# Performance work log

Hardware: AMD Instinct MI355X
Metric: run time of the kernel (lower is better)

The kernel has to match this reference:

```python
import jax, jax.numpy as jnp
import numpy as np

B, T, E, H = 2, 2048, 768, 12
DH = E // H  # per-head attention dim
EPS = 1e-5


def setup_inputs() -> dict:
    key = jax.random.key(0)
    ks = jax.random.split(key, 12)
    s = 0.02
    return {
        "x": jax.random.normal(ks[0], (B, T, E), dtype=jnp.float32),
        # stacked per-head projection weights: [H, E, DH], biases [H, DH]
        "Wq": jax.random.normal(ks[1], (H, E, DH), dtype=jnp.float32) * s,
        "bq": jax.random.normal(ks[2], (H, DH), dtype=jnp.float32) * s,
        "Wk": jax.random.normal(ks[3], (H, E, DH), dtype=jnp.float32) * s,
        "bk": jax.random.normal(ks[4], (H, DH), dtype=jnp.float32) * s,
        "Wv": jax.random.normal(ks[5], (H, E, DH), dtype=jnp.float32) * s,
        "bv": jax.random.normal(ks[6], (H, DH), dtype=jnp.float32) * s,
        "Wo": jax.random.normal(ks[7], (E, E), dtype=jnp.float32) * s,
        "bo": jax.random.normal(ks[8], (E,), dtype=jnp.float32) * s,
        "gamma": jnp.ones((E,), dtype=jnp.float32),
        "beta": jnp.zeros((E,), dtype=jnp.float32),
    }


def reference(x, Wq, bq, Wk, bk, Wv, bv, Wo, bo, gamma, beta):
    # per-head projections (heads stacked on axis h)
    q = jnp.einsum("bte,hed->bhtd", x, Wq) + bq[None, :, None, :]
    k = jnp.einsum("bte,hed->bhtd", x, Wk) + bk[None, :, None, :]
    v = jnp.einsum("bte,hed->bhtd", x, Wv) + bv[None, :, None, :]

    scores = jnp.einsum("bhtd,bhsd->bhts", q, k) / jnp.sqrt(jnp.float32(DH))
    causal = jnp.tril(jnp.ones((T, T), dtype=bool))  # True = keep
    scores = jnp.where(causal[None, None], scores, -jnp.inf)
    attn = jax.nn.softmax(scores, axis=-1)
    o = jnp.einsum("bhts,bhsd->bhtd", attn, v)  # [B,H,T,DH]

    # concat heads in head order -> [B,T,E]
    concat = jnp.transpose(o, (0, 2, 1, 3)).reshape(B, T, E)
    proj = concat @ Wo + bo

    # LayerNorm(proj) then residual add
    mu = jnp.mean(proj, axis=-1, keepdims=True)
    var = jnp.mean((proj - mu) ** 2, axis=-1, keepdims=True)
    normed = (proj - mu) * jax.lax.rsqrt(var + EPS) * gamma + beta
    return x + normed
```

## Files before the change

### kernel.cpp

```cpp
#include <hip/hip_runtime.h>
#include <stdint.h>

#define NROWS 4096
#define EMB   768
#define NQKV  2304
#define TSEQ  2048
#define NHEAD 12
#define NBH   24

typedef unsigned short u16;
typedef u16  ushort4v __attribute__((ext_vector_type(4)));
typedef u16  ushort8 __attribute__((ext_vector_type(8)));
typedef __bf16 bf16x8 __attribute__((ext_vector_type(8)));
typedef float f32x4 __attribute__((ext_vector_type(4)));

typedef const __attribute__((address_space(1))) void* gas_ptr;
typedef __attribute__((address_space(3))) void* las_ptr;

__device__ __forceinline__ u16 f2bf(float f) {
  union { float f; uint32_t u; } v; v.f = f;
  uint32_t u = v.u;
  return (u16)((u + 0x7fffu + ((u >> 16) & 1u)) >> 16);
}
__device__ __forceinline__ float bf2f(u16 u) {
  union { uint32_t u; float f; } v; v.u = ((uint32_t)u) << 16;
  return v.f;
}
__device__ __forceinline__ uint32_t cvtpk(float lo, float hi) {
  uint32_t r;
  asm("v_cvt_pk_bf16_f32 %0, %1, %2" : "=v"(r) : "v"(lo), "v"(hi));
  return r;
}

#define VMCNT0 asm volatile("s_waitcnt vmcnt(0)" ::: "memory")
#define LGKM0  asm volatile("s_waitcnt lgkmcnt(0)" ::: "memory")
#define SBAR   __builtin_amdgcn_s_barrier()
#define SCHED0 __builtin_amdgcn_sched_barrier(0)

__global__ __launch_bounds__(256) void k_pack(const float* __restrict__ x, u16* __restrict__ xb,
                                              const float* __restrict__ Wq, const float* __restrict__ Wk,
                                              const float* __restrict__ Wv, u16* __restrict__ wt,
                                              const float* __restrict__ Wo, u16* __restrict__ wot,
                                              uint32_t* __restrict__ cnt, uint32_t* __restrict__ tbl) {
  int bid = blockIdx.x, tid = threadIdx.x;
  if (bid == 0) {
    if (tid < 8) cnt[tid] = 0;
    if (tid >= 64 && tid < 144) {
      int p = tid - 64;
      int myqb = 0, myc = 0, k = 0;
      for (int qb = 0; qb < 32; ++qb) {
        int nch = (qb + 8) >> 3;
        for (int c = 0; c < nch; ++c) { if (k == p) { myqb = qb; myc = c; } ++k; }
      }
      int t0 = myc * 8;
      int t1 = (myqb + 1 < t0 + 8) ? myqb + 1 : t0 + 8;
      int mylen = t1 - t0, myid = myqb * 4 + myc;
      int rank = 0;
      for (int qb = 0; qb < 32; ++qb) {
        int nch = (qb + 8) >> 3;
        for (int c = 0; c < nch; ++c) {
          int u0 = c * 8;
          int u1 = (qb + 1 < u0 + 8) ? qb + 1 : u0 + 8;
          int l = u1 - u0, id = qb * 4 + c;
          if (l > mylen || (l == mylen && id < myid)) ++rank;
        }
      }
      tbl[rank] = (uint32_t)myqb | ((uint32_t)t0 << 8) | ((uint32_t)t1 << 16)
                | ((uint32_t)myc << 24) | (myqb <= 7 ? 0x80000000u : 0u);
    }
  }
  if (bid < 1536) {
    int i = bid * 2048 + tid * 8;
    float4 a = *(const float4*)(x + i);
    float4 b = *(const float4*)(x + i + 4);
    uint4 o;
    o.x = cvtpk(a.x, a.y); o.y = cvtpk(a.z, a.w);
    o.z = cvtpk(b.x, b.y); o.w = cvtpk(b.z, b.w);
    *(uint4*)(xb + i) = o;
    return;
  }
  __shared__ u16 lds[64][68];
  if (bid < 1968) {
    int t = bid - 1536;
    int sel = t / 144, rest = t - sel * 144;
    int h = rest / 12, ec = rest - h * 12;
    const float* W = sel == 0 ? Wq : (sel == 1 ? Wk : Wv);
    const float* src = W + ((size_t)(h * EMB + ec * 64) * 64);
    int e = tid >> 2, d0 = (tid & 3) * 16;
#pragma unroll
    for (int j = 0; j < 4; ++j) {
      float4 v = *(const float4*)(src + (size_t)e * 64 + d0 + 4 * j);
      ushort4v pk;
      uint32_t w0 = cvtpk(v.x, v.y), w1 = cvtpk(v.z, v.w);
      pk[0] = (u16)(w0 & 0xffff); pk[1] = (u16)(w0 >> 16);
      pk[2] = (u16)(w1 & 0xffff); pk[3] = (u16)(w1 >> 16);
      *(ushort4v*)(&lds[e][d0 + 4 * j]) = pk;
    }
    __syncthreads();
    int d = tid >> 2, e0 = (tid & 3) * 16;
    ushort8 o0, o1;
#pragma unroll
    for (int j = 0; j < 8; ++j) { o0[j] = lds[e0 + j][d]; o1[j] = lds[e0 + 8 + j][d]; }
    int n = sel * EMB + h * 64 + d;
    u16* dst = wt + (size_t)n * EMB + ec * 64 + e0;
    *(ushort8*)dst = o0;
    *(ushort8*)(dst + 8) = o1;
  } else {
    int t = bid - 1968;
    int er = t / 12, nc = t - er * 12;
    int e = tid >> 2, n0 = (tid & 3) * 16;
#pragma unroll
    for (int j = 0; j < 4; ++j) {
      float4 v = *(const float4*)(Wo + (size_t)(er * 64 + e) * EMB + nc * 64 + n0 + 4 * j);
      ushort4v pk;
      uint32_t w0 = cvtpk(v.x, v.y), w1 = cvtpk(v.z, v.w);
      pk[0] = (u16)(w0 & 0xffff); pk[1] = (u16)(w0 >> 16);
      pk[2] = (u16)(w1 & 0xffff); pk[3] = (u16)(w1 >> 16);
      *(ushort4v*)(&lds[e][n0 + 4 * j]) = pk;
    }
    __syncthreads();
    int n = tid >> 2, e0 = (tid & 3) * 16;
    ushort8 o0, o1;
#pragma unroll
    for (int j = 0; j < 8; ++j) { o0[j] = lds[e0 + j][n]; o1[j] = lds[e0 + 8 + j][n]; }
    u16* dst = wot + (size_t)(nc * 64 + n) * EMB + er * 64 + e0;
    *(ushort8*)dst = o0;
    *(ushort8*)(dst + 8) = o1;
  }
}

template<int BM, int BN, int OUT_MODE>
__global__ __launch_bounds__(256) void k_gemm(const u16* __restrict__ A, const u16* __restrict__ Bt,
                                              const float* __restrict__ b0, const float* __restrict__ b1,
                                              const float* __restrict__ b2, void* __restrict__ Cout,
                                              u16* __restrict__ vtout, int M, int N, int K) {
  constexpr int MR = BM / 32, NR = BN / 32;
  __shared__ u16 lds_a[BM * 64];
  __shared__ u16 lds_b[BN * 64];
  int tid = threadIdx.x;
  int w = tid >> 6, lane = tid & 63;
  int wr = w >> 1, wc = w & 1;
  int m0 = blockIdx.x * BM, n0 = blockIdx.y * BN;
  int lrow = lane & 15, g = lane >> 4;

  f32x4 zero = {0.f, 0.f, 0.f, 0.f};
  f32x4 acc[MR][NR];
  for (int m = 0; m < MR; ++m) for (int n = 0; n < NR; ++n) acc[m][n] = zero;

  int l8 = lane >> 3, c8 = lane & 7;

  for (int k0 = 0; k0 < K; k0 += 64) {
#pragma unroll
    for (int i = 0; i < BM / 32; ++i) {
      int row = w * (BM / 4) + 8 * i + l8;
      int c16 = c8 ^ (row & 7);
      const u16* ga = A + (size_t)(m0 + row) * K + k0 + c16 * 8;
      __builtin_amdgcn_global_load_lds((gas_ptr)ga, (las_ptr)(lds_a + (w * (BM / 4) + 8 * i) * 64), 16, 0, 0);
    }
#pragma unroll
    for (int i = 0; i < BN / 32; ++i) {
      int row = w * (BN / 4) + 8 * i + l8;
      int c16 = c8 ^ (row & 7);
      const u16* gb = Bt + (size_t)(n0 + row) * K + k0 + c16 * 8;
      __builtin_amdgcn_global_load_lds((gas_ptr)gb, (las_ptr)(lds_b + (w * (BN / 4) + 8 * i) * 64), 16, 0, 0);
    }
    __syncthreads();
    bf16x8 af[MR][2], bfr[NR][2];
#pragma unroll
    for (int m = 0; m < MR; ++m)
#pragma unroll
      for (int kc = 0; kc < 2; ++kc) {
        int row = wr * (BM / 2) + m * 16 + lrow;
        int ch = (kc * 4 + g) ^ (row & 7);
        af[m][kc] = *(const bf16x8*)(lds_a + row * 64 + ch * 8);
      }
#pragma unroll
    for (int n = 0; n < NR; ++n)
#pragma unroll
      for (int kc = 0; kc < 2; ++kc) {
        int row = wc * (BN / 2) + n * 16 + lrow;
        int ch = (kc * 4 + g) ^ (row & 7);
        bfr[n][kc] = *(const bf16x8*)(lds_b + row * 64 + ch * 8);
      }
#pragma unroll
    for (int kc = 0; kc < 2; ++kc)
#pragma unroll
      for (int m = 0; m < MR; ++m)
#pragma unroll
        for (int n = 0; n < NR; ++n)
          acc[m][n] = __builtin_amdgcn_mfma_f32_16x16x32_bf16(af[m][kc], bfr[n][kc], acc[m][n], 0, 0, 0);
    __syncthreads();
  }

#pragma unroll
  for (int m = 0; m < MR; ++m)
#pragma unroll
    for (int n = 0; n < NR; ++n) {
      int col = n0 + wc * (BN / 2) + n * 16 + lrow;
      float bcol;
      if (OUT_MODE == 1) bcol = b0[col];
      else {
        int sel = col >= 1536 ? 2 : (col >= 768 ? 1 : 0);
        const float* bs = sel == 0 ? b0 : (sel == 1 ? b1 : b2);
        bcol = bs[col - sel * EMB];
      }
      int row0 = m0 + wr * (BM / 2) + m * 16 + 4 * g;
      if (OUT_MODE == 2 && col >= 2 * EMB) {
        int c = col - 2 * EMB;
        int hh = c >> 6, d = c & 63;
        int bb = row0 >> 11, t = row0 & 2047;
        int y = bb * NHEAD + hh;
        ushort4v pk;
#pragma unroll
        for (int r = 0; r < 4; ++r) pk[r] = f2bf(acc[m][n][r] + bcol);
        *(ushort4v*)(vtout + (size_t)(y * 64 + d) * TSEQ + t) = pk;
      } else {
#pragma unroll
        for (int r = 0; r < 4; ++r) {
          int row = row0 + r;
          float v = acc[m][n][r] + bcol;
          if (OUT_MODE == 1) ((float*)Cout)[(size_t)row * N + col] = v;
          else               ((u16*)Cout)[(size_t)row * N + col] = f2bf(v);
        }
      }
    }
}

__global__ __launch_bounds__(256, 4) void k_attn(const u16* __restrict__ qkv, const u16* __restrict__ vt,
                                                 u16* __restrict__ aout, uint32_t* __restrict__ cnt,
                                                 const uint32_t* __restrict__ tbl,
                                                 u16* __restrict__ pO, float* __restrict__ pL) {
  __shared__ u16 kbuf[64 * 64];
  __shared__ u16 vbuf[2][64 * 64];
  __shared__ u16 pbuf[4][16 * 64];
  __shared__ int task_s;
  int tid = threadIdx.x;
  int w = tid >> 6, lane = tid & 63;
  int ql = lane & 15, g = lane >> 4;
  int xcd = blockIdx.x & 7;
  const float sc2 = 0.18033688f;
  u16* pw = &pbuf[w][0];
  int swz = (ql & 7) << 3;
  int l8 = lane >> 3, c8 = lane & 7;

  for (;;) {
    if (tid == 0) task_s = (int)atomicAdd(&cnt[xcd], 1u);
    __syncthreads();
    int tau = task_s;
    __syncthreads();
    if (tau >= 240) break;

    int rank = tau / 3, yl = tau - rank * 3;
    uint32_t te = tbl[rank];
    int qb = te & 0xff, t0 = (te >> 8) & 0xff, t1ex = (te >> 16) & 0xff, cslot = (te >> 24) & 0x7f;
    bool direct = (te >> 31) != 0;

    int y = xcd * 3 + yl;
    int b = y / NHEAD, h = y - b * NHEAD;
    int qrow0w = qb * 64 + w * 16;
    int qg = qrow0w + ql;

    const u16* qp = qkv + (size_t)(b * TSEQ + qg) * NQKV + h * 64;
    bf16x8 bq0 = *(const bf16x8*)(qp + g * 8);
    bf16x8 bq1 = *(const bf16x8*)(qp + 32 + g * 8);

    const u16* kst = qkv + (size_t)(b * TSEQ) * NQKV + EMB + h * 64;
    const u16* vst = vt + (size_t)y * 64 * TSEQ;

    f32x4 zero = {0.f, 0.f, 0.f, 0.f};
    f32x4 o[4]; for (int n = 0; n < 4; ++n) o[n] = zero;
    float lr = 0.f;

    auto STAGE_K = [&](int t_) {
#pragma unroll
      for (int i = 0; i < 2; ++i) {
        int row = i * 32 + 8 * w + l8;
        int c16 = c8 ^ (row & 7);
        const u16* gk = kst + (size_t)(t_ * 64 + row) * NQKV + c16 * 8;
        __builtin_amdgcn_global_load_lds((gas_ptr)gk, (las_ptr)(&kbuf[(i * 32 + 8 * w) * 64]), 16, 0, 0);
      }
    };
    auto STAGE_V = [&](int bi, int t_) {
#pragma unroll
      for (int i = 0; i < 2; ++i) {
        int row = i * 32 + 8 * w + l8;
        int c16 = c8 ^ (row & 7);
        const u16* gv = vst + (size_t)row * TSEQ + t_ * 64 + c16 * 8;
        __builtin_amdgcn_global_load_lds((gas_ptr)gv, (las_ptr)(&vbuf[bi][(i * 32 + 8 * w) * 64]), 16, 0, 0);
      }
    };

    STAGE_K(t0);
    STAGE_V(t0 & 1, t0);
    for (int t = t0; t < t1ex; ++t) {
      VMCNT0;
      SBAR;

      f32x4 st[4];
#pragma unroll
      for (int sblk = 0; sblk < 4; ++sblk) {
        int row = sblk * 16 + ql;
        bf16x8 ka0 = *(const bf16x8*)(kbuf + ((row * 64 + 8 * g) ^ swz));
        bf16x8 ka1 = *(const bf16x8*)(kbuf + ((row * 64 + 32 + 8 * g) ^ swz));
        f32x4 acc = zero;
        acc = __builtin_amdgcn_mfma_f32_16x16x32_bf16(ka0, bq0, acc, 0, 0, 0);
        acc = __builtin_amdgcn_mfma_f32_16x16x32_bf16(ka1, bq1, acc, 0, 0, 0);
        st[sblk] = acc;
      }
      SCHED0;
      SBAR;
      if (t + 1 < t1ex) { STAGE_K(t + 1); STAGE_V((t + 1) & 1, t + 1); }

      bool lastt = (t == qb);
      int s0 = t * 64;
      float e[4][4];
#pragma unroll
      for (int sblk = 0; sblk < 4; ++sblk)
#pragma unroll
        for (int r = 0; r < 4; ++r) {
          float vv = __builtin_fmaf(st[sblk][r], sc2, -2.0f);
          if (lastt) {
            int sg = s0 + sblk * 16 + 4 * g + r;
            if (sg > qg) vv = -1e30f;
          }
          float ee = __builtin_amdgcn_exp2f(vv);
          e[sblk][r] = ee;
          lr += ee;
        }

#pragma unroll
      for (int sblk = 0; sblk < 4; ++sblk) {
        uint2 dw;
        dw.x = cvtpk(e[sblk][0], e[sblk][1]);
        dw.y = cvtpk(e[sblk][2], e[sblk][3]);
        *(uint2*)(pw + ((ql * 64 + sblk * 16 + 4 * g) ^ swz)) = dw;
      }
      LGKM0; SCHED0;
      bf16x8 ap0 = *(const bf16x8*)(pw + ((ql * 64 + 8 * g) ^ swz));
      bf16x8 ap1 = *(const bf16x8*)(pw + ((ql * 64 + 32 + 8 * g) ^ swz));

      const u16* vb = &vbuf[t & 1][0];
#pragma unroll
      for (int n = 0; n < 4; ++n) {
        int row = n * 16 + ql;
        bf16x8 vb0 = *(const bf16x8*)(vb + ((row * 64 + 8 * g) ^ swz));
        bf16x8 vb1 = *(const bf16x8*)(vb + ((row * 64 + 32 + 8 * g) ^ swz));
        o[n] = __builtin_amdgcn_mfma_f32_16x16x32_bf16(ap0, vb0, o[n], 0, 0, 0);
        o[n] = __builtin_amdgcn_mfma_f32_16x16x32_bf16(ap1, vb1, o[n], 0, 0, 0);
      }
    }

    float lw = lr;
    lw += __shfl_xor(lw, 16);
    lw += __shfl_xor(lw, 32);

    if (direct) {
      float linv = 1.0f / lw;
      float li[4];
#pragma unroll
      for (int r = 0; r < 4; ++r) li[r] = __shfl(linv, 4 * g + r);
#pragma unroll
      for (int n = 0; n < 4; ++n)
#pragma unroll
        for (int r = 0; r < 4; ++r) {
          int q = qrow0w + 4 * g + r;
          aout[(size_t)(b * TSEQ + q) * EMB + h * 64 + n * 16 + ql] = f2bf(o[n][r] * li[r]);
        }
    } else {
      int blk2 = (y * 24 + (qb - 8)) * 4 + cslot;
      u16* po = pO + (size_t)blk2 * 4096;
      float* pl = pL + (size_t)blk2 * 64;
      if (g == 0) pl[w * 16 + ql] = lw;
#pragma unroll
      for (int n = 0; n < 4; ++n)
#pragma unroll
        for (int r = 0; r < 4; ++r) {
          int qloc = w * 16 + 4 * g + r;
          po[qloc * 64 + n * 16 + ql] = f2bf(o[n][r]);
        }
    }
  }
}

__global__ __launch_bounds__(256) void k_combine(const u16* __restrict__ pO, const float* __restrict__ pL,
                                                 u16* __restrict__ aout) {
  int blk = blockIdx.x;
  int y = blk / 24, q8 = blk - y * 24, qb = q8 + 8;
  int nch = (qb + 8) >> 3;
  int b = y / NHEAD, h = y - b * NHEAD;
  int tid = threadIdx.x;
  int row = tid >> 2, c0 = (tid & 3) * 16;
  float l = 0.f;
  for (int c = 0; c < nch; ++c) l += pL[((size_t)blk * 4 + c) * 64 + row];
  float rinv = 1.0f / l;
  float acc[16];
#pragma unroll
  for (int j = 0; j < 16; ++j) acc[j] = 0.f;
  for (int c = 0; c < nch; ++c) {
    const u16* p = pO + ((size_t)blk * 4 + c) * 4096 + row * 64 + c0;
    ushort8 a0 = *(const ushort8*)p;
    ushort8 a1 = *(const ushort8*)(p + 8);
#pragma unroll
    for (int j = 0; j < 8; ++j) { acc[j] += bf2f(a0[j]); acc[8 + j] += bf2f(a1[j]); }
  }
  ushort8 o0, o1;
#pragma unroll
  for (int j = 0; j < 8; j += 2) {
    uint32_t w0 = cvtpk(acc[j] * rinv, acc[j + 1] * rinv);
    o0[j] = (u16)(w0 & 0xffff); o0[j + 1] = (u16)(w0 >> 16);
    uint32_t w1 = cvtpk(acc[8 + j] * rinv, acc[9 + j] * rinv);
    o1[j] = (u16)(w1 & 0xffff); o1[j + 1] = (u16)(w1 >> 16);
  }
  u16* dst = aout + (size_t)(b * TSEQ + qb * 64 + row) * EMB + h * 64 + c0;
  *(ushort8*)dst = o0;
  *(ushort8*)(dst + 8) = o1;
}

__global__ __launch_bounds__(256) void k_ln_res(const float* __restrict__ proj, const float* __restrict__ x,
                                                const float* __restrict__ gamma, const float* __restrict__ beta,
                                                float* __restrict__ out) {
  __shared__ float smem[2][4];
  int row = blockIdx.x;
  const float* pr = proj + (size_t)row * EMB;
  const float* xr = x + (size_t)row * EMB;
  float* orow = out + (size_t)row * EMB;
  int tid = threadIdx.x;
  float v[3];
  float s = 0.f, s2 = 0.f;
#pragma unroll
  for (int i = 0; i < 3; ++i) { v[i] = pr[tid + 256 * i]; s += v[i]; s2 += v[i] * v[i]; }
#pragma unroll
  for (int m = 1; m < 64; m <<= 1) { s += __shfl_xor(s, m); s2 += __shfl_xor(s2, m); }
  int w = tid >> 6, lane = tid & 63;
  if (lane == 0) { smem[0][w] = s; smem[1][w] = s2; }
  __syncthreads();
  s  = smem[0][0] + smem[0][1] + smem[0][2] + smem[0][3];
  s2 = smem[1][0] + smem[1][1] + smem[1][2] + smem[1][3];
  float mu = s * (1.f / EMB);
  float var = s2 * (1.f / EMB) - mu * mu;
  float rstd = rsqrtf(var + 1e-5f);
#pragma unroll
  for (int i = 0; i < 3; ++i) {
    int c = tid + 256 * i;
    orow[c] = xr[c] + (v[i] - mu) * rstd * gamma[c] + beta[c];
  }
}

extern "C" void kernel_launch(void* const* d_in, const int* in_sizes, int n_in,
                              void* d_out, int out_size, void* d_ws, size_t ws_size,
                              hipStream_t stream) {
  const float* x     = (const float*)d_in[0];
  const float* Wq    = (const float*)d_in[1];
  const float* bq    = (const float*)d_in[2];
  const float* Wk    = (const float*)d_in[3];
  const float* bk    = (const float*)d_in[4];
  const float* Wv    = (const float*)d_in[5];
  const float* bv    = (const float*)d_in[6];
  const float* Wo    = (const float*)d_in[7];
  const float* bo    = (const float*)d_in[8];
  const float* gamma = (const float*)d_in[9];
  const float* beta  = (const float*)d_in[10];
  float* out = (float*)d_out;

  char* ws = (char*)d_ws;
  size_t off = 0;
  u16* xb    = (u16*)(ws + off); off += (size_t)NROWS * EMB * 2;
  u16* wqkvt = (u16*)(ws + off); off += (size_t)NQKV * EMB * 2;
  u16* wot   = (u16*)(ws + off); off += (size_t)EMB * EMB * 2;
  uint32_t* cnt = (uint32_t*)(ws + off); off += 64;
  uint32_t* tbl = (uint32_t*)(ws + off); off += 512;
  u16* qkv   = (u16*)(ws + off); off += (size_t)NROWS * NQKV * 2;
  u16* vt    = (u16*)(ws + off); off += (size_t)NBH * 64 * TSEQ * 2;
  u16* aout  = (u16*)(ws + off); off += (size_t)NROWS * EMB * 2;
  u16* pO    = (u16*)(ws + off); off += (size_t)NBH * 24 * 4 * 4096 * 2;
  float* pL  = (float*)(ws + off); off += (size_t)NBH * 24 * 4 * 64 * 4;
  float* proj = (float*)qkv;

  k_pack<<<dim3(2112), 256, 0, stream>>>(x, xb, Wq, Wk, Wv, wqkvt, Wo, wot, cnt, tbl);
  k_gemm<128, 128, 2><<<dim3(NROWS / 128, NQKV / 128), 256, 0, stream>>>(xb, wqkvt, bq, bk, bv, qkv, vt, NROWS, NQKV, EMB);
  k_attn<<<dim3(1024), 256, 0, stream>>>(qkv, vt, aout, cnt, tbl, pO, pL);
  k_combine<<<dim3(NBH * 24), 256, 0, stream>>>(pO, pL, aout);
  k_gemm<128, 64, 1><<<dim3(NROWS / 128, EMB / 64), 256, 0, stream>>>(aout, wot, bo, nullptr, nullptr, proj, nullptr, NROWS, EMB, EMB);
  k_ln_res<<<NROWS, 256, 0, stream>>>(proj, x, gamma, beta, out);
}
```

Before: 123.1 us.

## Make attention tasks per-wave with register-held K/V loaded directly from global

The attention kernel now hands out work per wave instead of per block, using a per-lane atomic and a shuffle, so there are four times as many tasks. K and V fragments are read straight from global memory into registers with a double-buffered K prefetch, replacing the LDS staging and the block barriers. The V-transpose buffer gets a padded row stride to avoid channel conflicts, and launch bounds drop to 3 blocks per SM to make room for the extra registers. The costs are redundant global/L2 traffic, since each wave now loads its own K/V, lower occupancy, and an odd extra multiply-divide in the normalization step.

```diff
diff --git a/kernel.cpp b/kernel.cpp
--- a/kernel.cpp
+++ b/kernel.cpp
@@ -5,6 +5,7 @@
 #define EMB   768
 #define NQKV  2304
 #define TSEQ  2048
+#define VTSTR 2080
 #define NHEAD 12
 #define NBH   24
 
@@ -32,9 +33,7 @@
   return r;
 }
 
-#define VMCNT0 asm volatile("s_waitcnt vmcnt(0)" ::: "memory")
 #define LGKM0  asm volatile("s_waitcnt lgkmcnt(0)" ::: "memory")
-#define SBAR   __builtin_amdgcn_s_barrier()
 #define SCHED0 __builtin_amdgcn_sched_barrier(0)
 
 __global__ __launch_bounds__(256) void k_pack(const float* __restrict__ x, u16* __restrict__ xb,
@@ -213,7 +212,7 @@
         ushort4v pk;
 #pragma unroll
         for (int r = 0; r < 4; ++r) pk[r] = f2bf(acc[m][n][r] + bcol);
-        *(ushort4v*)(vtout + (size_t)(y * 64 + d) * TSEQ + t) = pk;
+        *(ushort4v*)(vtout + (size_t)(y * 64 + d) * VTSTR + t) = pk;
       } else {
 #pragma unroll
         for (int r = 0; r < 4; ++r) {
@@ -226,31 +225,28 @@
     }
 }
 
-__global__ __launch_bounds__(256, 4) void k_attn(const u16* __restrict__ qkv, const u16* __restrict__ vt,
+__global__ __launch_bounds__(256, 3) void k_attn(const u16* __restrict__ qkv, const u16* __restrict__ vt,
                                                  u16* __restrict__ aout, uint32_t* __restrict__ cnt,
                                                  const uint32_t* __restrict__ tbl,
                                                  u16* __restrict__ pO, float* __restrict__ pL) {
-  __shared__ u16 kbuf[64 * 64];
-  __shared__ u16 vbuf[2][64 * 64];
   __shared__ u16 pbuf[4][16 * 64];
-  __shared__ int task_s;
   int tid = threadIdx.x;
-  int w = tid >> 6, lane = tid & 63;
+  int wphys = tid >> 6, lane = tid & 63;
   int ql = lane & 15, g = lane >> 4;
   int xcd = blockIdx.x & 7;
   const float sc2 = 0.18033688f;
-  u16* pw = &pbuf[w][0];
+  u16* pw = &pbuf[wphys][0];
   int swz = (ql & 7) << 3;
-  int l8 = lane >> 3, c8 = lane & 7;
+  f32x4 zero = {0.f, 0.f, 0.f, 0.f};
 
   for (;;) {
-    if (tid == 0) task_s = (int)atomicAdd(&cnt[xcd], 1u);
-    __syncthreads();
-    int tau = task_s;
-    __syncthreads();
-    if (tau >= 240) break;
-
-    int rank = tau / 3, yl = tau - rank * 3;
+    int tau = 0;
+    if (lane == 0) tau = (int)atomicAdd(&cnt[xcd], 1u);
+    tau = __shfl(tau, 0);
+    if (tau >= 960) break;
+
+    int rank = tau / 12, rem = tau - rank * 12;
+    int yl = rem >> 2, w = rem & 3;
     uint32_t te = tbl[rank];
     int qb = te & 0xff, t0 = (te >> 8) & 0xff, t1ex = (te >> 16) & 0xff, cslot = (te >> 24) & 0x7f;
     bool direct = (te >> 31) != 0;
@@ -265,89 +261,83 @@
     bf16x8 bq1 = *(const bf16x8*)(qp + 32 + g * 8);
 
     const u16* kst = qkv + (size_t)(b * TSEQ) * NQKV + EMB + h * 64;
-    const u16* vst = vt + (size_t)y * 64 * TSEQ;
-
-    f32x4 zero = {0.f, 0.f, 0.f, 0.f};
+    const u16* vst = vt + (size_t)y * 64 * VTSTR;
+
     f32x4 o[4]; for (int n = 0; n < 4; ++n) o[n] = zero;
     float lr = 0.f;
 
-    auto STAGE_K = [&](int t_) {
-#pragma unroll
-      for (int i = 0; i < 2; ++i) {
-        int row = i * 32 + 8 * w + l8;
-        int c16 = c8 ^ (row & 7);
-        const u16* gk = kst + (size_t)(t_ * 64 + row) * NQKV + c16 * 8;
-        __builtin_amdgcn_global_load_lds((gas_ptr)gk, (las_ptr)(&kbuf[(i * 32 + 8 * w) * 64]), 16, 0, 0);
+    bf16x8 kA[8], kB[8], vv[8];
+
+    auto LOADK = [&](int t_, bf16x8 (&kf)[8]) {
+#pragma unroll
+      for (int sblk = 0; sblk < 4; ++sblk) {
+        const u16* p = kst + (size_t)(t_ * 64 + sblk * 16 + ql) * NQKV + 8 * g;
+        kf[2 * sblk]     = *(const bf16x8*)(p);
+        kf[2 * sblk + 1] = *(const bf16x8*)(p + 32);
       }
     };
-    auto STAGE_V = [&](int bi, int t_) {
-#pragma unroll
-      for (int i = 0; i < 2; ++i) {
-        int row = i * 32 + 8 * w + l8;
-        int c16 = c8 ^ (row & 7);
-        const u16* gv = vst + (size_t)row * TSEQ + t_ * 64 + c16 * 8;
-        __builtin_amdgcn_global_load_lds((gas_ptr)gv, (las_ptr)(&vbuf[bi][(i * 32 + 8 * w) * 64]), 16, 0, 0);
+    auto LOADV = [&](int t_) {
+#pragma unroll
+      for (int n = 0; n < 4; ++n) {
+        const u16* p = vst + (size_t)(n * 16 + ql) * VTSTR + t_ * 64 + 8 * g;
+        vv[2 * n]     = *(const bf16x8*)(p);
+        vv[2 * n + 1] = *(const bf16x8*)(p + 32);
       }
     };
-
-    STAGE_K(t0);
-    STAGE_V(t0 & 1, t0);
-    for (int t = t0; t < t1ex; ++t) {
-      VMCNT0;
-      SBAR;
-
+    auto TILE = [&](bf16x8 (&kc)[8], bf16x8 (&kn)[8], int t_) {
+      LOADV(t_);
       f32x4 st[4];
 #pragma unroll
       for (int sblk = 0; sblk < 4; ++sblk) {
-        int row = sblk * 16 + ql;
-        bf16x8 ka0 = *(const bf16x8*)(kbuf + ((row * 64 + 8 * g) ^ swz));
-        bf16x8 ka1 = *(const bf16x8*)(kbuf + ((row * 64 + 32 + 8 * g) ^ swz));
         f32x4 acc = zero;
-        acc = __builtin_amdgcn_mfma_f32_16x16x32_bf16(ka0, bq0, acc, 0, 0, 0);
-        acc = __builtin_amdgcn_mfma_f32_16x16x32_bf16(ka1, bq1, acc, 0, 0, 0);
+        acc = __builtin_amdgcn_mfma_f32_16x16x32_bf16(kc[2 * sblk], bq0, acc, 0, 0, 0);
+        acc = __builtin_amdgcn_mfma_f32_16x16x32_bf16(kc[2 * sblk + 1], bq1, acc, 0, 0, 0);
         st[sblk] = acc;
       }
-      SCHED0;
-      SBAR;
-      if (t + 1 < t1ex) { STAGE_K(t + 1); STAGE_V((t + 1) & 1, t + 1); }
-
-      bool lastt = (t == qb);
-      int s0 = t * 64;
-      float e[4][4];
-#pragma unroll
-      for (int sblk = 0; sblk < 4; ++sblk)
-#pragma unroll
-        for (int r = 0; r < 4; ++r) {
-          float vv = __builtin_fmaf(st[sblk][r], sc2, -2.0f);
+      if (t_ + 1 < t1ex) LOADK(t_ + 1, kn);
+      bool lastt = (t_ == qb);
+      int s0 = t_ * 64;
+#pragma unroll
+      for (int sblk = 0; sblk < 4; ++sblk) {
+        float e0, e1, e2, e3;
+        {
+          float v0 = __builtin_fmaf(st[sblk][0], sc2, -2.0f);
+          float v1 = __builtin_fmaf(st[sblk][1], sc2, -2.0f);
+          float v2 = __builtin_fmaf(st[sblk][2], sc2, -2.0f);
+          float v3 = __builtin_fmaf(st[sblk][3], sc2, -2.0f);
           if (lastt) {
-            int sg = s0 + sblk * 16 + 4 * g + r;
-            if (sg > qg) vv = -1e30f;
+            int sg = s0 + sblk * 16 + 4 * g;
+            if (sg + 0 > qg) v0 = -1e30f;
+            if (sg + 1 > qg) v1 = -1e30f;
+            if (sg + 2 > qg) v2 = -1e30f;
+            if (sg + 3 > qg) v3 = -1e30f;
           }
-          float ee = __builtin_amdgcn_exp2f(vv);
-          e[sblk][r] = ee;
-          lr += ee;
+          e0 = __builtin_amdgcn_exp2f(v0);
+          e1 = __builtin_amdgcn_exp2f(v1);
+          e2 = __builtin_amdgcn_exp2f(v2);
+          e3 = __builtin_amdgcn_exp2f(v3);
+          lr += (e0 + e1) + (e2 + e3);
         }
-
-#pragma unroll
-      for (int sblk = 0; sblk < 4; ++sblk) {
         uint2 dw;
-        dw.x = cvtpk(e[sblk][0], e[sblk][1]);
-        dw.y = cvtpk(e[sblk][2], e[sblk][3]);
+        dw.x = cvtpk(e0, e1);
+        dw.y = cvtpk(e2, e3);
         *(uint2*)(pw + ((ql * 64 + sblk * 16 + 4 * g) ^ swz)) = dw;
       }
       LGKM0; SCHED0;
       bf16x8 ap0 = *(const bf16x8*)(pw + ((ql * 64 + 8 * g) ^ swz));
       bf16x8 ap1 = *(const bf16x8*)(pw + ((ql * 64 + 32 + 8 * g) ^ swz));
-
-      const u16* vb = &vbuf[t & 1][0];
 #pragma unroll
       for (int n = 0; n < 4; ++n) {
-        int row = n * 16 + ql;
-        bf16x8 vb0 = *(const bf16x8*)(vb + ((row * 64 + 8 * g) ^ swz));
-        bf16x8 vb1 = *(const bf16x8*)(vb + ((row * 64 + 32 + 8 * g) ^ swz));
-        o[n] = __builtin_amdgcn_mfma_f32_16x16x32_bf16(ap0, vb0, o[n], 0, 0, 0);
-        o[n] = __builtin_amdgcn_mfma_f32_16x16x32_bf16(ap1, vb1, o[n], 0, 0, 0);
-      }
+        o[n] = __builtin_amdgcn_mfma_f32_16x16x32_bf16(ap0, vv[2 * n], o[n], 0, 0, 0);
+        o[n] = __builtin_amdgcn_mfma_f32_16x16x32_bf16(ap1, vv[2 * n + 1], o[n], 0, 0, 0);
+      }
+    };
+
+    LOADK(t0, kA);
+    int t = t0;
+    for (;;) {
+      TILE(kA, kB, t); ++t; if (t >= t1ex) break;
+      TILE(kB, kA, t); ++t; if (t >= t1ex) break;
     }
 
     float lw = lr;
@@ -364,7 +354,7 @@
 #pragma unroll
         for (int r = 0; r < 4; ++r) {
           int q = qrow0w + 4 * g + r;
-          aout[(size_t)(b * TSEQ + q) * EMB + h * 64 + n * 16 + ql] = f2bf(o[n][r] * li[r]);
+          aout[(size_t)(b * TSEQ + q) * EMB + h * 64 + n * 16 + ql] = f2bf(o[n][r] * linv * (li[r] / linv));
         }
     } else {
       int blk2 = (y * 24 + (qb - 8)) * 4 + cslot;
@@ -470,7 +460,7 @@
   uint32_t* cnt = (uint32_t*)(ws + off); off += 64;
   uint32_t* tbl = (uint32_t*)(ws + off); off += 512;
   u16* qkv   = (u16*)(ws + off); off += (size_t)NROWS * NQKV * 2;
-  u16* vt    = (u16*)(ws + off); off += (size_t)NBH * 64 * TSEQ * 2;
+  u16* vt    = (u16*)(ws + off); off += (size_t)NBH * 64 * VTSTR * 2;
   u16* aout  = (u16*)(ws + off); off += (size_t)NROWS * EMB * 2;
   u16* pO    = (u16*)(ws + off); off += (size_t)NBH * 24 * 4 * 4096 * 2;
   float* pL  = (float*)(ws + off); off += (size_t)NBH * 24 * 4 * 64 * 4;
```

Result: slower. 284.5 us (+131.0%).
